# Kernel optimization log

Measured on AMD Instinct MI355X. Metric: run time of the kernel, lower is better.

Reference implementation:

```python
import jax, jax.numpy as jnp
import numpy as np

B, L, D, H, W, LBL = 256, 512, 32, 128, 256, 10

# Tsit5 explicit tableau (Tsitouras 2011), fixed-step variant (no error estimate)
C2, C3, C4, C5, C6 = 0.161, 0.327, 0.9, 0.9800255409045097, 1.0
A21 = 0.161
A31, A32 = -0.008480655492356989, 0.335480655492357
A41, A42, A43 = 2.8971530571054935, -6.359448489975075, 4.3622954328695815
A51, A52, A53, A54 = 5.325864828439257, -11.748883564062828, 7.4955393428898365, -0.09249506636175525
A61, A62, A63, A64, A65 = 5.86145544294642, -12.92096931784711, 8.159367898576159, -0.071584973281401, -0.028269050394068383
B1, B2, B3, B4, B5, B6 = 0.09646076681806523, 0.01, 0.4798896504144996, 1.379008574103742, -3.290069515436081, 2.324710524099774


def setup_inputs() -> dict:
    key = jax.random.key(0)
    ks = jax.random.split(key, 16)
    sc = 0.1  # keep control path smooth / well-scaled
    return {
        "ts": jnp.linspace(0.0, 1.0, L, dtype=jnp.float32),
        "coeff_d": jax.random.normal(ks[0], (B, L - 1, D), jnp.float32) * sc,
        "coeff_c": jax.random.normal(ks[1], (B, L - 1, D), jnp.float32) * sc,
        "coeff_b": jax.random.normal(ks[2], (B, L - 1, D), jnp.float32) * sc,
        "coeff_a": jax.random.normal(ks[3], (B, L - 1, D), jnp.float32) * sc,
        "x0": jax.random.normal(ks[4], (B, D), jnp.float32),
        "l1_w": jax.random.normal(ks[5], (H, D), jnp.float32) / np.float32(np.sqrt(D)),
        "l1_b": jax.random.normal(ks[6], (H,), jnp.float32) * 0.01,
        "mlp_w0": jax.random.normal(ks[7], (W, H), jnp.float32) / np.float32(np.sqrt(H)),
        "mlp_b0": jax.random.normal(ks[8], (W,), jnp.float32) * 0.01,
        "mlp_w1": jax.random.normal(ks[9], (W, W), jnp.float32) / np.float32(np.sqrt(W)),
        "mlp_b1": jax.random.normal(ks[10], (W,), jnp.float32) * 0.01,
        "mlp_w2": jax.random.normal(ks[11], (H * D, W), jnp.float32) / np.float32(np.sqrt(W)),
        "mlp_b2": jax.random.normal(ks[12], (H * D,), jnp.float32) * 0.01,
        "l2_w": jax.random.normal(ks[13], (LBL, H), jnp.float32) / np.float32(np.sqrt(H)),
        "l2_b": jax.random.normal(ks[14], (LBL,), jnp.float32) * 0.01,
    }


def reference(ts, coeff_d, coeff_c, coeff_b, coeff_a, x0,
              l1_w, l1_b, mlp_w0, mlp_b0, mlp_w1, mlp_b1, mlp_w2, mlp_b2,
              l2_w, l2_b):
    Bn, Dd = x0.shape
    Hh = l1_w.shape[0]

    def vf(y):  # (B,H) -> (B,H,D); MLP with silu hiddens, tanh final
        h = jax.nn.silu(y @ mlp_w0.T + mlp_b0)
        h = jax.nn.silu(h @ mlp_w1.T + mlp_b1)
        return jnp.tanh(h @ mlp_w2.T + mlp_b2).reshape(Bn, Hh, Dd)

    def rhs(y, frac, cd, cc, cb):
        # cubic Hermite control derivative dX/dt at local offset frac within interval
        dX = cb + frac * (2.0 * cc + 3.0 * frac * cd)  # (B,D)
        return jnp.einsum('bhd,bd->bh', vf(y), dX)

    y0 = x0 @ l1_w.T + l1_b  # (B,H)
    dts = ts[1:] - ts[:-1]  # (L-1,)
    cdT = jnp.transpose(coeff_d, (1, 0, 2))  # (L-1,B,D)
    ccT = jnp.transpose(coeff_c, (1, 0, 2))
    cbT = jnp.transpose(coeff_b, (1, 0, 2))

    def step(y, xs):
        h, cd, cc, cb = xs
        k1 = rhs(y, 0.0, cd, cc, cb)
        k2 = rhs(y + h * (A21 * k1), C2 * h, cd, cc, cb)
        k3 = rhs(y + h * (A31 * k1 + A32 * k2), C3 * h, cd, cc, cb)
        k4 = rhs(y + h * (A41 * k1 + A42 * k2 + A43 * k3), C4 * h, cd, cc, cb)
        k5 = rhs(y + h * (A51 * k1 + A52 * k2 + A53 * k3 + A54 * k4), C5 * h, cd, cc, cb)
        k6 = rhs(y + h * (A61 * k1 + A62 * k2 + A63 * k3 + A64 * k4 + A65 * k5), C6 * h, cd, cc, cb)
        y_new = y + h * (B1 * k1 + B2 * k2 + B3 * k3 + B4 * k4 + B5 * k5 + B6 * k6)
        return y_new, None

    yT, _ = jax.lax.scan(step, y0, (dts, cdT, ccT, cbT))
    return jax.nn.softmax(yT @ l2_w.T + l2_b, axis=-1)  # (B, label_dim)
```

## Files before the change

### kernel.cpp

```cpp
#include <hip/hip_runtime.h>

typedef unsigned int u32;
typedef unsigned long long u64;
typedef unsigned short u16;
typedef __attribute__((ext_vector_type(8))) short bf16x8;
typedef __attribute__((ext_vector_type(4))) float f32x4;
typedef __attribute__((ext_vector_type(4))) u32 u32x4;

static constexpr int NWG    = 256;
static constexpr int NTHR   = 256;
static constexpr int NSTEPS = 511;

static constexpr size_t K_OFF   = 0;
static constexpr size_t KG_U32  = 6ull * 16 * 16 * 64;
static constexpr size_t W0_OFF  = KG_U32 * 4;
static constexpr size_t W1_OFF  = W0_OFF + 256 * 128 * 2;
static constexpr size_t W2_OFF  = W1_OFF + 256 * 256 * 2;
static constexpr size_t WS_NEED = W2_OFF + 4096ull * 256 * 2;

static constexpr float AT6c[6][6] = {
  {0.f, 0.f, 0.f, 0.f, 0.f, 0.f},
  {0.161f, 0.f, 0.f, 0.f, 0.f, 0.f},
  {-0.008480655492356989f, 0.335480655492357f, 0.f, 0.f, 0.f, 0.f},
  {2.8971530571054935f, -6.359448489975075f, 4.3622954328695815f, 0.f, 0.f, 0.f},
  {5.325864828439257f, -11.748883564062828f, 7.4955393428898365f, -0.09249506636175525f, 0.f, 0.f},
  {5.86145544294642f, -12.92096931784711f, 8.159367898576159f, -0.071584973281401f, -0.028269050394068383f, 0.f}
};
static constexpr float BT6c[6] = {
  0.09646076681806523f, 0.01f, 0.4798896504144996f, 1.379008574103742f,
  -3.290069515436081f, 2.324710524099774f
};
static constexpr float CT6c[6] = {0.f, 0.161f, 0.327f, 0.9f, 0.9800255409045097f, 1.f};

__device__ __forceinline__ u16 cvbf(float f) {
  u32 u = __float_as_uint(f);
  return (u16)((u + 0x7fffu + ((u >> 16) & 1u)) >> 16);
}
__device__ __forceinline__ u32 cvt_pk(float lo, float hi) {
  u32 r;
  asm("v_cvt_pk_bf16_f32 %0, %1, %2" : "=v"(r) : "v"(lo), "v"(hi));
  return r;
}
__device__ __forceinline__ float blo(u32 u) { return __uint_as_float(u << 16); }
__device__ __forceinline__ float bhi(u32 u) { return __uint_as_float(u & 0xffff0000u); }
__device__ __forceinline__ float frcp(float x) { return __builtin_amdgcn_rcpf(x); }
__device__ __forceinline__ float fsilu(float x) { return x * frcp(1.f + __expf(-x)); }
__device__ __forceinline__ float ftanh(float x) { return 1.f - 2.f * frcp(__expf(2.f * x) + 1.f); }
__device__ __forceinline__ f32x4 MF(bf16x8 a, bf16x8 b, f32x4 c) {
  return __builtin_amdgcn_mfma_f32_16x16x32_bf16(a, b, c, 0, 0, 0);
}

__global__ void cvt_weights(const float* __restrict__ w0, const float* __restrict__ w1,
                            const float* __restrict__ w2, u16* __restrict__ o0,
                            u16* __restrict__ o1, u16* __restrict__ o2) {
  int i = blockIdx.x * blockDim.x + threadIdx.x;
  if (i < 256 * 128)  o0[i] = cvbf(w0[i]);
  if (i < 256 * 256)  o1[i] = cvbf(w1[i]);
  if (i < 4096 * 256) o2[i] = cvbf(w2[i]);
}

__launch_bounds__(NTHR, 1)
__global__ void cde_kernel(const float* __restrict__ ts,
                           const float* __restrict__ cdg, const float* __restrict__ ccg,
                           const float* __restrict__ cbg,
                           const float* __restrict__ x0g, const float* __restrict__ l1w,
                           const float* __restrict__ l1b,
                           const float* __restrict__ b0g, const float* __restrict__ b1g,
                           const float* __restrict__ b2g,
                           const float* __restrict__ l2w, const float* __restrict__ l2b,
                           const u16* __restrict__ w0b, const u16* __restrict__ w1b,
                           const u16* __restrict__ w2b,
                           u32* kg, float* __restrict__ outp) {
  __shared__ u32 w2l[32768];
  __shared__ u16 ysl[16 * 128];
  __shared__ u16 h1l[16 * 256];
  __shared__ u16 h2l[16 * 256];
  __shared__ float dxt[32 * 17];
  __shared__ float lg[192];
  __shared__ u32 kex[1024] __attribute__((aligned(16)));

  const int t  = threadIdx.x;
  const int wg = blockIdx.x;
  const int g  = wg >> 4;
  const int hs = wg & 15;
  const int b0r = g * 16;
  const int wv = t >> 6, l = t & 63, lr = l & 15, lk = l >> 4;
  const int row_o = t & 15;
  const int hb    = (t >> 4) * 8;

  bf16x8 w0f[4][4], w1f[4][8];
  float bias0v[4], bias1v[4], bias2v[4];
#pragma unroll
  for (int ct = 0; ct < 4; ++ct) {
    const int col = wv * 64 + ct * 16 + lr;
    bias0v[ct] = b0g[col];
    bias1v[ct] = b1g[col];
    bias2v[ct] = b2g[hs * 256 + col];
    const u16* base0 = w0b + (size_t)col * 128 + lk * 8;
#pragma unroll
    for (int ks = 0; ks < 4; ++ks) w0f[ct][ks] = *(const bf16x8*)(base0 + ks * 32);
    const u16* base1 = w1b + (size_t)col * 256 + lk * 8;
#pragma unroll
    for (int ks = 0; ks < 8; ++ks) w1f[ct][ks] = *(const bf16x8*)(base1 + ks * 32);
    const u16* base2 = w2b + (size_t)(hs * 256 + col) * 256 + lk * 8;
#pragma unroll
    for (int ks = 0; ks < 8; ++ks) {
      u32x4 v = *(const u32x4*)(base2 + ks * 32);
      *(u32x4*)&w2l[(size_t)((ks * 16 + wv * 4 + ct) * 64 + l) * 4] = v;
    }
  }

  float yv[8];
  {
    const float* xr = x0g + (size_t)(b0r + row_o) * 32;
#pragma unroll
    for (int e = 0; e < 8; ++e) {
      float acc = l1b[hb + e];
      const float* wr = l1w + (size_t)(hb + e) * 32;
#pragma unroll
      for (int d = 0; d < 32; ++d) acc = fmaf(xr[d], wr[d], acc);
      yv[e] = acc;
    }
  }

  u32 kk[6][4];
#pragma unroll
  for (int j = 0; j < 6; ++j)
#pragma unroll
    for (int p = 0; p < 4; ++p) kk[j][p] = 0u;

  float pcb[2], pcc[2], pcd[2];
  auto ld_coeff = [&](int st) {
    size_t gi = ((size_t)(b0r + (t >> 4)) * 511 + st) * 32 + 2 * (t & 15);
    float2 vb = *(const float2*)(cbg + gi); pcb[0] = vb.x; pcb[1] = vb.y;
    float2 vc = *(const float2*)(ccg + gi); pcc[0] = vc.x; pcc[1] = vc.y;
    float2 vd = *(const float2*)(cdg + gi); pcd[0] = vd.x; pcd[1] = vd.y;
  };
  ld_coeff(0);
  float hh_next = ts[1] - ts[0];
  const size_t myoff = (size_t)((t >> 4) * 64 + (t & 15) * 4);
  __syncthreads();

#pragma unroll 1
  for (int step = 0; step < NSTEPS; ++step) {
    const float hh = hh_next;
    const float cb0 = pcb[0], cb1 = pcb[1];
    const float cc0 = pcc[0], cc1 = pcc[1];
    const float cd0 = pcd[0], cd1 = pcd[1];
    if (step + 1 < NSTEPS) { ld_coeff(step + 1); hh_next = ts[step + 2] - ts[step + 1]; }
    const u32 tg = (u32)(step + 1) & 3u;
    const u32 tgins = (tg & 1u) | ((tg & 2u) << 15);

    auto spin_gather = [&](int sdone, u32 (&kks)[4]) {
      const u64* p = (const u64*)(kg + (size_t)((sdone * 16 + g) * 16) * 64 + myoff);
      u64 a, b;
      for (;;) {
        a = __hip_atomic_load(p,     __ATOMIC_RELAXED, __HIP_MEMORY_SCOPE_AGENT);
        b = __hip_atomic_load(p + 1, __ATOMIC_RELAXED, __HIP_MEMORY_SCOPE_AGENT);
        u32 a0 = (u32)a, a1 = (u32)(a >> 32), b0 = (u32)b, b1 = (u32)(b >> 32);
        u32 t0 = (a0 & 1u) | ((a0 >> 15) & 2u);
        u32 t1 = (a1 & 1u) | ((a1 >> 15) & 2u);
        u32 t2 = (b0 & 1u) | ((b0 >> 15) & 2u);
        u32 t3 = (b1 & 1u) | ((b1 >> 15) & 2u);
        if (((t0 ^ tg) | (t1 ^ tg) | (t2 ^ tg) | (t3 ^ tg)) == 0u) break;
      }
      kks[0] = (u32)a; kks[1] = (u32)(a >> 32); kks[2] = (u32)b; kks[3] = (u32)(b >> 32);
    };

    auto run = [&](int s) {
      const float fr = CT6c[s] * hh;
      {
        int d0 = 2 * (t & 15), rl = t >> 4;
        dxt[d0 * 17 + rl]       = cb0 + fr * (2.f * cc0 + 3.f * fr * cd0);
        dxt[(d0 + 1) * 17 + rl] = cb1 + fr * (2.f * cc1 + 3.f * fr * cd1);
      }
      {
        u32 yp[4];
#pragma unroll
        for (int p = 0; p < 4; ++p) {
          float v0 = yv[2 * p], v1 = yv[2 * p + 1];
          for (int j = 0; j < s; ++j) {
            const float aj = hh * AT6c[s][j];
            v0 = fmaf(aj, blo(kk[j][p]), v0);
            v1 = fmaf(aj, bhi(kk[j][p]), v1);
          }
          yp[p] = cvt_pk(v0, v1);
        }
        int boff = row_o * 256 + (((t >> 4) * 16) ^ ((row_o & 7) << 4));
        u32x4 w; w[0] = yp[0]; w[1] = yp[1]; w[2] = yp[2]; w[3] = yp[3];
        *(u32x4*)((char*)ysl + boff) = w;
      }
      __syncthreads();

      f32x4 acc[4];
#pragma unroll
      for (int ct = 0; ct < 4; ++ct) acc[ct] = f32x4{0.f, 0.f, 0.f, 0.f};
#pragma unroll
      for (int ks = 0; ks < 4; ++ks) {
        bf16x8 af = *(const bf16x8*)((char*)ysl + lr * 256 + ((ks * 64 + lk * 16) ^ ((lr & 7) << 4)));
#pragma unroll
        for (int ct = 0; ct < 4; ++ct) acc[ct] = MF(af, w0f[ct][ks], acc[ct]);
      }
#pragma unroll
      for (int ct = 0; ct < 4; ++ct) {
        int col2 = (wv * 64 + ct * 16 + lr) * 2;
        int r0 = lk * 4;
        u32 p01 = cvt_pk(fsilu(acc[ct][0] + bias0v[ct]), fsilu(acc[ct][1] + bias0v[ct]));
        u32 p23 = cvt_pk(fsilu(acc[ct][2] + bias0v[ct]), fsilu(acc[ct][3] + bias0v[ct]));
        *(u16*)((char*)h1l + (r0 + 0) * 512 + (col2 ^ (((r0 + 0) & 7) << 4))) = (u16)p01;
        *(u16*)((char*)h1l + (r0 + 1) * 512 + (col2 ^ (((r0 + 1) & 7) << 4))) = (u16)(p01 >> 16);
        *(u16*)((char*)h1l + (r0 + 2) * 512 + (col2 ^ (((r0 + 2) & 7) << 4))) = (u16)p23;
        *(u16*)((char*)h1l + (r0 + 3) * 512 + (col2 ^ (((r0 + 3) & 7) << 4))) = (u16)(p23 >> 16);
      }
      __syncthreads();

#pragma unroll
      for (int ct = 0; ct < 4; ++ct) acc[ct] = f32x4{0.f, 0.f, 0.f, 0.f};
#pragma unroll
      for (int ks = 0; ks < 8; ++ks) {
        bf16x8 af = *(const bf16x8*)((char*)h1l + lr * 512 + ((ks * 64 + lk * 16) ^ ((lr & 7) << 4)));
#pragma unroll
        for (int ct = 0; ct < 4; ++ct) acc[ct] = MF(af, w1f[ct][ks], acc[ct]);
      }
#pragma unroll
      for (int ct = 0; ct < 4; ++ct) {
        int col2 = (wv * 64 + ct * 16 + lr) * 2;
        int r0 = lk * 4;
        u32 p01 = cvt_pk(fsilu(acc[ct][0] + bias1v[ct]), fsilu(acc[ct][1] + bias1v[ct]));
        u32 p23 = cvt_pk(fsilu(acc[ct][2] + bias1v[ct]), fsilu(acc[ct][3] + bias1v[ct]));
        *(u16*)((char*)h2l + (r0 + 0) * 512 + (col2 ^ (((r0 + 0) & 7) << 4))) = (u16)p01;
        *(u16*)((char*)h2l + (r0 + 1) * 512 + (col2 ^ (((r0 + 1) & 7) << 4))) = (u16)(p01 >> 16);
        *(u16*)((char*)h2l + (r0 + 2) * 512 + (col2 ^ (((r0 + 2) & 7) << 4))) = (u16)p23;
        *(u16*)((char*)h2l + (r0 + 3) * 512 + (col2 ^ (((r0 + 3) & 7) << 4))) = (u16)(p23 >> 16);
      }
      __syncthreads();

#pragma unroll
      for (int ct = 0; ct < 4; ++ct) acc[ct] = f32x4{0.f, 0.f, 0.f, 0.f};
#pragma unroll
      for (int ks = 0; ks < 8; ++ks) {
        bf16x8 af = *(const bf16x8*)((char*)h2l + lr * 512 + ((ks * 64 + lk * 16) ^ ((lr & 7) << 4)));
#pragma unroll
        for (int ct = 0; ct < 4; ++ct) {
          bf16x8 bf = *(const bf16x8*)&w2l[(size_t)((ks * 16 + wv * 4 + ct) * 64 + l) * 4];
          acc[ct] = MF(af, bf, acc[ct]);
        }
      }
      {
        float s01[4], s23[4];
#pragma unroll
        for (int r = 0; r < 4; ++r) {
          int row = lk * 4 + r;
          float v0 = ftanh(acc[0][r] + bias2v[0]) * dxt[lr * 17 + row];
          float v1 = ftanh(acc[1][r] + bias2v[1]) * dxt[(16 + lr) * 17 + row];
          s01[r] = v0 + v1;
          float v2 = ftanh(acc[2][r] + bias2v[2]) * dxt[lr * 17 + row];
          float v3 = ftanh(acc[3][r] + bias2v[3]) * dxt[(16 + lr) * 17 + row];
          s23[r] = v2 + v3;
        }
#pragma unroll
        for (int m = 1; m < 16; m <<= 1) {
#pragma unroll
          for (int r = 0; r < 4; ++r) {
            s01[r] += __shfl_xor(s01[r], m, 64);
            s23[r] += __shfl_xor(s23[r], m, 64);
          }
        }
        if (lr == 0) {
#pragma unroll
          for (int r = 0; r < 4; ++r)
            kex[(lk * 4 + r) * 4 + wv] = cvt_pk(s01[r], s23[r]);
        }
      }
      __syncthreads();
      const size_t slab = (size_t)((s * 16 + g) * 16 + hs) * 64;
      if (wv == 0) {
        u32 val = (kex[l] & 0xFFFEFFFEu) | tgins;
        __hip_atomic_store(&kg[slab + l], val, __ATOMIC_RELAXED, __HIP_MEMORY_SCOPE_AGENT);
      }
    };

#pragma unroll
    for (int s = 0; s < 6; ++s) {
      if (s > 0) spin_gather(s - 1, kk[s - 1]);
      run(s);
    }
    spin_gather(5, kk[5]);

#pragma unroll
    for (int p = 0; p < 4; ++p) {
      float v0 = yv[2 * p], v1 = yv[2 * p + 1];
#pragma unroll
      for (int j = 0; j < 6; ++j) {
        const float cj = hh * BT6c[j];
        v0 = fmaf(cj, blo(kk[j][p]), v0);
        v1 = fmaf(cj, bhi(kk[j][p]), v1);
      }
      yv[2 * p] = v0; yv[2 * p + 1] = v1;
    }
  }

  __syncthreads();
  if (hs == 0) {
    float* yh = (float*)w2l;
#pragma unroll
    for (int e = 0; e < 8; ++e) yh[row_o * 132 + hb + e] = yv[e];
    __syncthreads();
    if (t < 160) {
      int r = t / 10, c = t - r * 10;
      float acc = l2b[c];
      const float* wr = l2w + (size_t)c * 128;
      for (int h2 = 0; h2 < 128; ++h2) acc = fmaf(yh[r * 132 + h2], wr[h2], acc);
      lg[r * 12 + c] = acc;
    }
    __syncthreads();
    if (t < 16) {
      float m = lg[t * 12];
#pragma unroll
      for (int c = 1; c < 10; ++c) m = fmaxf(m, lg[t * 12 + c]);
      float sum = 0.f, ex[10];
#pragma unroll
      for (int c = 0; c < 10; ++c) { ex[c] = __expf(lg[t * 12 + c] - m); sum += ex[c]; }
      float inv = 1.f / sum;
#pragma unroll
      for (int c = 0; c < 10; ++c) outp[(size_t)(b0r + t) * 10 + c] = ex[c] * inv;
    }
  }
}

extern "C" void kernel_launch(void* const* d_in, const int* in_sizes, int n_in,
                              void* d_out, int out_size, void* d_ws, size_t ws_size,
                              hipStream_t stream) {
  (void)in_sizes; (void)n_in; (void)out_size;
  if (ws_size < WS_NEED) return;

  const float* ts  = (const float*)d_in[0];
  const float* cd  = (const float*)d_in[1];
  const float* cc  = (const float*)d_in[2];
  const float* cb  = (const float*)d_in[3];
  const float* x0  = (const float*)d_in[5];
  const float* l1w = (const float*)d_in[6];
  const float* l1b = (const float*)d_in[7];
  const float* w0  = (const float*)d_in[8];
  const float* b0  = (const float*)d_in[9];
  const float* w1  = (const float*)d_in[10];
  const float* b1  = (const float*)d_in[11];
  const float* w2  = (const float*)d_in[12];
  const float* b2  = (const float*)d_in[13];
  const float* l2w = (const float*)d_in[14];
  const float* l2b = (const float*)d_in[15];

  char* ws = (char*)d_ws;
  u32* kg  = (u32*)(ws + K_OFF);
  u16* w0b = (u16*)(ws + W0_OFF);
  u16* w1b = (u16*)(ws + W1_OFF);
  u16* w2b = (u16*)(ws + W2_OFF);

  (void)hipMemsetAsync(kg, 0x01, KG_U32 * 4, stream);
  cvt_weights<<<4096, 256, 0, stream>>>(w0, w1, w2, w0b, w1b, w2b);
  cde_kernel<<<NWG, NTHR, 0, stream>>>(ts, cd, cc, cb, x0, l1w, l1b,
                                       b0, b1, b2, l2w, l2b,
                                       w0b, w1b, w2b, kg, (float*)d_out);
}
```

Measured before the change: 14.98 ms.

## Double block to 512 threads, splitting each MLP wave's columns in half

Raises the persistent kernel's workgroup from 4 to 8 waves. Each wave now computes 32 output columns (2 MFMA tiles) instead of 64 in all three MLP layers. The state update, coefficient loads and spin gathers stay on the first 256 threads. The aim is to shorten the per-stage MLP critical path and cut register pressure per wave. The cost is more barrier participants, idle waves during the spin waits, and a packed-u16 exchange layout whose correctness depends on the indexing.

New measurement: 12.19 ms, median of 3. 1.23x faster.

```diff
diff --git a/kernel.cpp b/kernel.cpp
--- a/kernel.cpp
+++ b/kernel.cpp
@@ -8,7 +8,7 @@
 typedef __attribute__((ext_vector_type(4))) u32 u32x4;
 
 static constexpr int NWG    = 256;
-static constexpr int NTHR   = 256;
+static constexpr int NTHR   = 512;
 static constexpr int NSTEPS = 511;
 
 static constexpr size_t K_OFF   = 0;
@@ -59,7 +59,7 @@
   if (i < 4096 * 256) o2[i] = cvbf(w2[i]);
 }
 
-__launch_bounds__(NTHR, 1)
+__launch_bounds__(NTHR)
 __global__ void cde_kernel(const float* __restrict__ ts,
                            const float* __restrict__ cdg, const float* __restrict__ ccg,
                            const float* __restrict__ cbg,
@@ -77,22 +77,23 @@
   __shared__ u16 h2l[16 * 256];
   __shared__ float dxt[32 * 17];
   __shared__ float lg[192];
-  __shared__ u32 kex[1024] __attribute__((aligned(16)));
+  __shared__ u32 kexw[64];
 
   const int t  = threadIdx.x;
   const int wg = blockIdx.x;
   const int g  = wg >> 4;
   const int hs = wg & 15;
   const int b0r = g * 16;
-  const int wv = t >> 6, l = t & 63, lr = l & 15, lk = l >> 4;
+  const int w = t >> 6, l = t & 63, lr = l & 15, lk = l >> 4;
   const int row_o = t & 15;
-  const int hb    = (t >> 4) * 8;
-
-  bf16x8 w0f[4][4], w1f[4][8];
-  float bias0v[4], bias1v[4], bias2v[4];
-#pragma unroll
-  for (int ct = 0; ct < 4; ++ct) {
-    const int col = wv * 64 + ct * 16 + lr;
+  const int hb    = ((t >> 4) & 15) * 8;
+  const bool act  = (t < 256);
+
+  bf16x8 w0f[2][4], w1f[2][8];
+  float bias0v[2], bias1v[2], bias2v[2];
+#pragma unroll
+  for (int ct = 0; ct < 2; ++ct) {
+    const int col = w * 32 + ct * 16 + lr;
     bias0v[ct] = b0g[col];
     bias1v[ct] = b1g[col];
     bias2v[ct] = b2g[hs * 256 + col];
@@ -106,7 +107,7 @@
 #pragma unroll
     for (int ks = 0; ks < 8; ++ks) {
       u32x4 v = *(const u32x4*)(base2 + ks * 32);
-      *(u32x4*)&w2l[(size_t)((ks * 16 + wv * 4 + ct) * 64 + l) * 4] = v;
+      *(u32x4*)&w2l[(size_t)((ks * 16 + (w * 2 + ct)) * 64 + l) * 4] = v;
     }
   }
 
@@ -131,11 +132,13 @@
 
   float pcb[2], pcc[2], pcd[2];
   auto ld_coeff = [&](int st) {
+    if (!act) return;
     size_t gi = ((size_t)(b0r + (t >> 4)) * 511 + st) * 32 + 2 * (t & 15);
     float2 vb = *(const float2*)(cbg + gi); pcb[0] = vb.x; pcb[1] = vb.y;
     float2 vc = *(const float2*)(ccg + gi); pcc[0] = vc.x; pcc[1] = vc.y;
     float2 vd = *(const float2*)(cdg + gi); pcd[0] = vd.x; pcd[1] = vd.y;
   };
+  pcb[0]=pcb[1]=pcc[0]=pcc[1]=pcd[0]=pcd[1]=0.f;
   ld_coeff(0);
   float hh_next = ts[1] - ts[0];
   const size_t myoff = (size_t)((t >> 4) * 64 + (t & 15) * 4);
@@ -152,6 +155,7 @@
     const u32 tgins = (tg & 1u) | ((tg & 2u) << 15);
 
     auto spin_gather = [&](int sdone, u32 (&kks)[4]) {
+      if (!act) return;
       const u64* p = (const u64*)(kg + (size_t)((sdone * 16 + g) * 16) * 64 + myoff);
       u64 a, b;
       for (;;) {
@@ -168,13 +172,11 @@
     };
 
     auto run = [&](int s) {
-      const float fr = CT6c[s] * hh;
-      {
+      if (act) {
+        const float fr = CT6c[s] * hh;
         int d0 = 2 * (t & 15), rl = t >> 4;
         dxt[d0 * 17 + rl]       = cb0 + fr * (2.f * cc0 + 3.f * fr * cd0);
         dxt[(d0 + 1) * 17 + rl] = cb1 + fr * (2.f * cc1 + 3.f * fr * cd1);
-      }
-      {
         u32 yp[4];
 #pragma unroll
         for (int p = 0; p < 4; ++p) {
@@ -186,24 +188,24 @@
           }
           yp[p] = cvt_pk(v0, v1);
         }
-        int boff = row_o * 256 + (((t >> 4) * 16) ^ ((row_o & 7) << 4));
-        u32x4 w; w[0] = yp[0]; w[1] = yp[1]; w[2] = yp[2]; w[3] = yp[3];
-        *(u32x4*)((char*)ysl + boff) = w;
+        int boff = row_o * 256 + ((((t >> 4) & 15) * 16) ^ ((row_o & 7) << 4));
+        u32x4 wv_; wv_[0] = yp[0]; wv_[1] = yp[1]; wv_[2] = yp[2]; wv_[3] = yp[3];
+        *(u32x4*)((char*)ysl + boff) = wv_;
       }
       __syncthreads();
 
-      f32x4 acc[4];
-#pragma unroll
-      for (int ct = 0; ct < 4; ++ct) acc[ct] = f32x4{0.f, 0.f, 0.f, 0.f};
+      f32x4 acc[2];
+#pragma unroll
+      for (int ct = 0; ct < 2; ++ct) acc[ct] = f32x4{0.f, 0.f, 0.f, 0.f};
 #pragma unroll
       for (int ks = 0; ks < 4; ++ks) {
         bf16x8 af = *(const bf16x8*)((char*)ysl + lr * 256 + ((ks * 64 + lk * 16) ^ ((lr & 7) << 4)));
 #pragma unroll
-        for (int ct = 0; ct < 4; ++ct) acc[ct] = MF(af, w0f[ct][ks], acc[ct]);
-      }
-#pragma unroll
-      for (int ct = 0; ct < 4; ++ct) {
-        int col2 = (wv * 64 + ct * 16 + lr) * 2;
+        for (int ct = 0; ct < 2; ++ct) acc[ct] = MF(af, w0f[ct][ks], acc[ct]);
+      }
+#pragma unroll
+      for (int ct = 0; ct < 2; ++ct) {
+        int col2 = (w * 32 + ct * 16 + lr) * 2;
         int r0 = lk * 4;
         u32 p01 = cvt_pk(fsilu(acc[ct][0] + bias0v[ct]), fsilu(acc[ct][1] + bias0v[ct]));
         u32 p23 = cvt_pk(fsilu(acc[ct][2] + bias0v[ct]), fsilu(acc[ct][3] + bias0v[ct]));
@@ -215,16 +217,16 @@
       __syncthreads();
 
 #pragma unroll
-      for (int ct = 0; ct < 4; ++ct) acc[ct] = f32x4{0.f, 0.f, 0.f, 0.f};
+      for (int ct = 0; ct < 2; ++ct) acc[ct] = f32x4{0.f, 0.f, 0.f, 0.f};
 #pragma unroll
       for (int ks = 0; ks < 8; ++ks) {
         bf16x8 af = *(const bf16x8*)((char*)h1l + lr * 512 + ((ks * 64 + lk * 16) ^ ((lr & 7) << 4)));
 #pragma unroll
-        for (int ct = 0; ct < 4; ++ct) acc[ct] = MF(af, w1f[ct][ks], acc[ct]);
-      }
-#pragma unroll
-      for (int ct = 0; ct < 4; ++ct) {
-        int col2 = (wv * 64 + ct * 16 + lr) * 2;
+        for (int ct = 0; ct < 2; ++ct) acc[ct] = MF(af, w1f[ct][ks], acc[ct]);
+      }
+#pragma unroll
+      for (int ct = 0; ct < 2; ++ct) {
+        int col2 = (w * 32 + ct * 16 + lr) * 2;
         int r0 = lk * 4;
         u32 p01 = cvt_pk(fsilu(acc[ct][0] + bias1v[ct]), fsilu(acc[ct][1] + bias1v[ct]));
         u32 p23 = cvt_pk(fsilu(acc[ct][2] + bias1v[ct]), fsilu(acc[ct][3] + bias1v[ct]));
@@ -236,46 +238,39 @@
       __syncthreads();
 
 #pragma unroll
-      for (int ct = 0; ct < 4; ++ct) acc[ct] = f32x4{0.f, 0.f, 0.f, 0.f};
+      for (int ct = 0; ct < 2; ++ct) acc[ct] = f32x4{0.f, 0.f, 0.f, 0.f};
 #pragma unroll
       for (int ks = 0; ks < 8; ++ks) {
         bf16x8 af = *(const bf16x8*)((char*)h2l + lr * 512 + ((ks * 64 + lk * 16) ^ ((lr & 7) << 4)));
 #pragma unroll
-        for (int ct = 0; ct < 4; ++ct) {
-          bf16x8 bf = *(const bf16x8*)&w2l[(size_t)((ks * 16 + wv * 4 + ct) * 64 + l) * 4];
+        for (int ct = 0; ct < 2; ++ct) {
+          bf16x8 bf = *(const bf16x8*)&w2l[(size_t)((ks * 16 + (w * 2 + ct)) * 64 + l) * 4];
           acc[ct] = MF(af, bf, acc[ct]);
         }
       }
       {
-        float s01[4], s23[4];
+        float sv[4];
 #pragma unroll
         for (int r = 0; r < 4; ++r) {
           int row = lk * 4 + r;
-          float v0 = ftanh(acc[0][r] + bias2v[0]) * dxt[lr * 17 + row];
-          float v1 = ftanh(acc[1][r] + bias2v[1]) * dxt[(16 + lr) * 17 + row];
-          s01[r] = v0 + v1;
-          float v2 = ftanh(acc[2][r] + bias2v[2]) * dxt[lr * 17 + row];
-          float v3 = ftanh(acc[3][r] + bias2v[3]) * dxt[(16 + lr) * 17 + row];
-          s23[r] = v2 + v3;
+          sv[r] = ftanh(acc[0][r] + bias2v[0]) * dxt[lr * 17 + row] +
+                  ftanh(acc[1][r] + bias2v[1]) * dxt[(16 + lr) * 17 + row];
         }
 #pragma unroll
         for (int m = 1; m < 16; m <<= 1) {
 #pragma unroll
-          for (int r = 0; r < 4; ++r) {
-            s01[r] += __shfl_xor(s01[r], m, 64);
-            s23[r] += __shfl_xor(s23[r], m, 64);
-          }
+          for (int r = 0; r < 4; ++r) sv[r] += __shfl_xor(sv[r], m, 64);
         }
         if (lr == 0) {
 #pragma unroll
           for (int r = 0; r < 4; ++r)
-            kex[(lk * 4 + r) * 4 + wv] = cvt_pk(s01[r], s23[r]);
+            *((u16*)kexw + (lk * 4 + r) * 8 + w) = (u16)cvt_pk(sv[r], sv[r]);
         }
       }
       __syncthreads();
       const size_t slab = (size_t)((s * 16 + g) * 16 + hs) * 64;
-      if (wv == 0) {
-        u32 val = (kex[l] & 0xFFFEFFFEu) | tgins;
+      if (t < 64) {
+        u32 val = (kexw[l] & 0xFFFEFFFEu) | tgins;
         __hip_atomic_store(&kg[slab + l], val, __ATOMIC_RELAXED, __HIP_MEMORY_SCOPE_AGENT);
       }
     };
@@ -303,8 +298,10 @@
   __syncthreads();
   if (hs == 0) {
     float* yh = (float*)w2l;
-#pragma unroll
-    for (int e = 0; e < 8; ++e) yh[row_o * 132 + hb + e] = yv[e];
+    if (act) {
+#pragma unroll
+      for (int e = 0; e < 8; ++e) yh[row_o * 132 + hb + e] = yv[e];
+    }
     __syncthreads();
     if (t < 160) {
       int r = t / 10, c = t - r * 10;
```
